# Kernel optimization log

Hardware: AMD Instinct MI355X
Metric: run time of the kernel (lower is better)

The kernel has to match this reference:

```python
import jax, jax.numpy as jnp
import numpy as np

B, N, D, H = 2, 2048, 1024, 16
HD = D // H

def setup_inputs() -> dict:
    key = jax.random.key(0)
    ks = jax.random.split(key, 8)
    s = lambda fan_in: 1.0 / np.sqrt(fan_in)
    return {
        "x": jax.random.normal(ks[0], (B, N, D), jnp.float32),
        "coverage": jax.random.uniform(ks[1], (B, N, 1), jnp.float32),
        "w_qkv": jax.random.normal(ks[2], (D, 3 * D), jnp.float32) * s(D),
        "w_out": jax.random.normal(ks[3], (D, D), jnp.float32) * s(D),
        "b_out": jnp.zeros((D,), jnp.float32),
        "w_ce1": jax.random.normal(ks[4], (1, D // 4), jnp.float32),
        "b_ce1": jnp.zeros((D // 4,), jnp.float32),
        "w_ce2": jax.random.normal(ks[5], (D // 4, H), jnp.float32) * s(D // 4),
        "b_ce2": jnp.zeros((H,), jnp.float32),
        "w_fg1": jax.random.normal(ks[6], (D, D // 4), jnp.float32) * s(D),
        "b_fg1": jnp.zeros((D // 4,), jnp.float32),
        "w_fg2": jax.random.normal(ks[7], (D // 4, 1), jnp.float32) * s(D // 4),
        "b_fg2": jnp.zeros((1,), jnp.float32),
    }

def reference(x, coverage, w_qkv, w_out, b_out, w_ce1, b_ce1, w_ce2, b_ce2,
              w_fg1, b_fg1, w_fg2, b_fg2):
    b, n, d = x.shape
    h = w_ce2.shape[1]
    hd = d // h
    scale = hd ** -0.5
    qkv = x @ w_qkv  # (B,N,3D)
    q, k, v = jnp.split(qkv, 3, axis=-1)
    q = q.reshape(b, n, h, hd).transpose(0, 2, 1, 3)  # (B,H,N,hd)
    k = k.reshape(b, n, h, hd).transpose(0, 2, 1, 3)
    v = v.reshape(b, n, h, hd).transpose(0, 2, 1, 3)
    attn = jnp.einsum("bhnd,bhmd->bhnm", q, k) * scale  # (B,H,N,N)
    # coverage bias: MLP(1 -> D/4 -> H), broadcast over query dim
    cov = jax.nn.silu(coverage @ w_ce1 + b_ce1) @ w_ce2 + b_ce2  # (B,N,H)
    cov_bias = cov.transpose(0, 2, 1)[:, :, None, :]  # (B,H,1,N)
    # fusion gate on mean-pooled features
    x_pooled = x.mean(axis=1)  # (B,D)
    g = jax.nn.sigmoid(jax.nn.silu(x_pooled @ w_fg1 + b_fg1) @ w_fg2 + b_fg2)  # (B,1)
    g = g[:, :, None, None]  # (B,1,1,1)
    # g*(attn+bias) + (1-g)*attn == attn + g*bias (exact same math)
    attn = attn + g * cov_bias
    attn = jax.nn.softmax(attn, axis=-1)
    out = jnp.einsum("bhnm,bhmd->bhnd", attn, v)  # (B,H,N,hd)
    out = out.transpose(0, 2, 1, 3).reshape(b, n, d)
    return out @ w_out + b_out
```

## Files before the change

### kernel.cpp

```cpp
#include <hip/hip_runtime.h>
#include <math.h>

typedef __bf16 bf16_t;
typedef __bf16 bf16x8 __attribute__((ext_vector_type(8)));
typedef __bf16 bf16x4 __attribute__((ext_vector_type(4)));
typedef float f32x4 __attribute__((ext_vector_type(4)));

#define MFMA16(a, b, c) __builtin_amdgcn_mfma_f32_16x16x32_bf16((a), (b), (c), 0, 0, 0)

constexpr int Bc = 2, Nc = 2048, Dc = 1024, Hc = 16, HDc = 64;
constexpr float C1 = 0.18033688011112042f;
constexpr float LOG2E = 1.4426950408889634f;

__device__ __forceinline__ void glds16(const bf16_t* g, bf16_t* l) {
    __builtin_amdgcn_global_load_lds(
        (const __attribute__((address_space(1))) unsigned int*)g,
        (__attribute__((address_space(3))) unsigned int*)l, 16, 0, 0);
}

__device__ __forceinline__ void glds4(const float* g, float* l) {
    __builtin_amdgcn_global_load_lds(
        (const __attribute__((address_space(1))) unsigned int*)g,
        (__attribute__((address_space(3))) unsigned int*)l, 4, 0, 0);
}

__global__ __launch_bounds__(256) void f2b(const float* __restrict__ src,
                                           bf16_t* __restrict__ dst) {
    int i = (blockIdx.x * 256 + threadIdx.x) * 4;
    float4 v = *(const float4*)(src + i);
    bf16x4 o = { (bf16_t)v.x, (bf16_t)v.y, (bf16_t)v.z, (bf16_t)v.w };
    *(bf16x4*)(dst + i) = o;
}

__global__ __launch_bounds__(256) void tr64(const float* __restrict__ src,
                                            bf16_t* __restrict__ dst, int R, int C) {
    __shared__ bf16_t tile[64 * 66];
    int r0 = blockIdx.y * 64, c0 = blockIdx.x * 64;
    int t = threadIdx.x;
    int cl = t & 63, rl = t >> 6;
#pragma unroll
    for (int p = 0; p < 16; ++p) {
        int r = p * 4 + rl;
        tile[r * 66 + cl] = (bf16_t)src[(size_t)(r0 + r) * C + c0 + cl];
    }
    __syncthreads();
#pragma unroll
    for (int p = 0; p < 16; ++p) {
        int r = p * 4 + rl;
        dst[(size_t)(c0 + r) * R + r0 + cl] = tile[cl * 66 + r];
    }
}

__global__ __launch_bounds__(256) void pool_partial(const float* __restrict__ x,
                                                    float* __restrict__ pooled) {
    int blk = blockIdx.x;
    int b = blk >> 7, ch = blk & 127;
    int t = threadIdx.x;
    int c = t * 4;
    float s0 = 0.f, s1 = 0.f, s2 = 0.f, s3 = 0.f;
    for (int rr = 0; rr < 16; ++rr) {
        float4 v = *(const float4*)(x + (size_t)(b * Nc + ch * 16 + rr) * Dc + c);
        s0 += v.x; s1 += v.y; s2 += v.z; s3 += v.w;
    }
    atomicAdd(&pooled[b * Dc + c + 0], s0);
    atomicAdd(&pooled[b * Dc + c + 1], s1);
    atomicAdd(&pooled[b * Dc + c + 2], s2);
    atomicAdd(&pooled[b * Dc + c + 3], s3);
}

__global__ __launch_bounds__(256) void gate1(const float* __restrict__ pooled,
                                             const float* __restrict__ w_fg1,
                                             const float* __restrict__ b_fg1,
                                             const float* __restrict__ w_fg2,
                                             float* __restrict__ hacc) {
    int b = blockIdx.x >> 8, j = blockIdx.x & 255;
    int t = threadIdx.x;
    float p = 0.f;
#pragma unroll
    for (int i = 0; i < 4; ++i) {
        int d = t * 4 + i;
        p += pooled[b * 1024 + d] * w_fg1[d * 256 + j];
    }
#pragma unroll
    for (int off = 32; off > 0; off >>= 1) p += __shfl_down(p, off);
    __shared__ float red[4];
    if ((t & 63) == 0) red[t >> 6] = p;
    __syncthreads();
    if (t == 0) {
        float hj = (red[0] + red[1] + red[2] + red[3]) * (1.0f / 2048.0f) + b_fg1[j];
        hj = hj / (1.0f + __expf(-hj));
        atomicAdd(&hacc[b], hj * w_fg2[j]);
    }
}

__global__ __launch_bounds__(256) void covbias_k(const float* __restrict__ coverage,
                                                 const float* __restrict__ w_ce1,
                                                 const float* __restrict__ b_ce1,
                                                 const float* __restrict__ w_ce2,
                                                 const float* __restrict__ b_ce2,
                                                 const float* __restrict__ hacc,
                                                 const float* __restrict__ b_fg2,
                                                 float* __restrict__ biasbuf) {
    int t = threadIdx.x;
    int h = t & 15;
    int gn = blockIdx.x * 16 + (t >> 4);
    int b = gn >> 11, n = gn & 2047;
    float g = 1.0f / (1.0f + __expf(-(hacc[b] + b_fg2[0])));
    float c = coverage[gn];
    float acc = b_ce2[h];
    for (int j = 0; j < 256; ++j) {
        float tv = c * w_ce1[j] + b_ce1[j];
        tv = tv / (1.0f + __expf(-tv));
        acc += tv * w_ce2[j * 16 + h];
    }
    biasbuf[((size_t)b * 16 + h) * 2048 + n] = LOG2E * g * acc;
}

__global__ __launch_bounds__(256) void qkv_gemm(const bf16_t* __restrict__ Xb,
                                                const bf16_t* __restrict__ Wt,
                                                bf16_t* __restrict__ Q,
                                                bf16_t* __restrict__ Kb,
                                                bf16_t* __restrict__ Vt) {
    __shared__ __align__(16) bf16_t At[128 * 32];
    __shared__ __align__(16) bf16_t Bt[128 * 32];
    int t = threadIdx.x, w = t >> 6, lane = t & 63;
    int l16 = lane & 15, quad = lane >> 4;
    int wm = w & 1, wx = w >> 1;
    int m0 = blockIdx.x * 128;
    int n0 = blockIdx.y * 128;
    f32x4 acc[4][4] = {};
    int sw = (l16 >> 2) & 3;

    for (int k0 = 0; k0 < 1024; k0 += 32) {
#pragma unroll
        for (int i = 0; i < 2; ++i) {
            int fb = i * 4096 + w * 1024;
            int f = fb + lane * 16;
            int row = f >> 6;
            int ch = (f >> 4) & 3;
            int sc = ch ^ ((row >> 2) & 3);
            glds16(Wt + (size_t)(n0 + row) * 1024 + k0 + sc * 8, At + (fb >> 1));
            glds16(Xb + (size_t)(m0 + row) * 1024 + k0 + sc * 8, Bt + (fb >> 1));
        }
        __syncthreads();
        bf16x8 afr[4], bfr[4];
#pragma unroll
        for (int mi = 0; mi < 4; ++mi)
            afr[mi] = *(const bf16x8*)(At + (wm * 64 + mi * 16 + l16) * 32 + ((quad ^ sw) * 8));
#pragma unroll
        for (int ni = 0; ni < 4; ++ni)
            bfr[ni] = *(const bf16x8*)(Bt + (wx * 64 + ni * 16 + l16) * 32 + ((quad ^ sw) * 8));
#pragma unroll
        for (int mi = 0; mi < 4; ++mi)
#pragma unroll
            for (int ni = 0; ni < 4; ++ni)
                acc[mi][ni] = MFMA16(afr[mi], bfr[ni], acc[mi][ni]);
        __syncthreads();
    }

    int sec = n0 >> 10;
    float scq = (sec == 0) ? C1 : 1.0f;
#pragma unroll
    for (int mi = 0; mi < 4; ++mi) {
        int gc = n0 + wm * 64 + mi * 16 + quad * 4;
        int dcol = gc & 1023;
        int h = dcol >> 6, hd = dcol & 63;
#pragma unroll
        for (int ni = 0; ni < 4; ++ni) {
            int gx = m0 + wx * 64 + ni * 16 + l16;
            int b = gx >> 11, n = gx & 2047;
            size_t bh = (size_t)(b * 16 + h);
            if (sec == 2) {
#pragma unroll
                for (int r = 0; r < 4; ++r)
                    Vt[(bh * 64 + hd + r) * 2048 + n] = (bf16_t)acc[mi][ni][r];
            } else {
                bf16x4 pk = { (bf16_t)(acc[mi][ni][0] * scq), (bf16_t)(acc[mi][ni][1] * scq),
                              (bf16_t)(acc[mi][ni][2] * scq), (bf16_t)(acc[mi][ni][3] * scq) };
                bf16_t* dst = (sec == 0 ? Q : Kb);
                *(bf16x4*)(dst + (bh * 2048 + n) * 64 + hd) = pk;
            }
        }
    }
}

__global__ __launch_bounds__(256) void attn_k(const bf16_t* __restrict__ Q,
                                              const bf16_t* __restrict__ Kb,
                                              const bf16_t* __restrict__ Vt,
                                              const float* __restrict__ biasbuf,
                                              bf16_t* __restrict__ O) {
    __shared__ __align__(16) bf16_t kbuf[2][64 * 64];
    __shared__ __align__(16) bf16_t vbuf[2][64 * 64];
    __shared__ __align__(16) float bbias[2][64];
    int t = threadIdx.x, w = t >> 6, lane = t & 63;
    int l16 = lane & 15, quad = lane >> 4;
    int bh = blockIdx.y;
    int b = bh >> 4, h = bh & 15;
    int qa = blockIdx.x * 128 + w * 32;
    const bf16_t* Qh = Q + (size_t)bh * 2048 * 64;
    const bf16_t* Kh = Kb + (size_t)bh * 2048 * 64;
    const bf16_t* Vh = Vt + (size_t)bh * 64 * 2048;
    const float* bih = biasbuf + (size_t)bh * 2048;

    int fb0 = w * 2048, fb1 = fb0 + 1024;
    int f0 = fb0 + lane * 16, f1 = fb1 + lane * 16;
    int krow0 = f0 >> 7, kch0 = ((f0 >> 4) & 7) ^ (krow0 & 7);
    int krow1 = f1 >> 7, kch1 = ((f1 >> 4) & 7) ^ (krow1 & 7);

    bf16x8 qf[2][2];
#pragma unroll
    for (int qt = 0; qt < 2; ++qt)
#pragma unroll
        for (int dh = 0; dh < 2; ++dh)
            qf[qt][dh] = *(const bf16x8*)(Qh + (size_t)(qa + qt * 16 + l16) * 64 + dh * 32 + quad * 8);

    f32x4 o[2][4] = {};
    f32x4 lacc[2] = {};
    bf16x8 onesb;
#pragma unroll
    for (int i = 0; i < 8; ++i) onesb[i] = (bf16_t)1.0f;
    int swl = l16 & 7;
    int qh = quad >> 1, ql = quad & 1;

    auto stage = [&](int tile, int bf) {
        int jn = tile * 64;
        glds16(Kh + (size_t)(jn + krow0) * 64 + kch0 * 8, &kbuf[bf][fb0 >> 1]);
        glds16(Kh + (size_t)(jn + krow1) * 64 + kch1 * 8, &kbuf[bf][fb1 >> 1]);
        glds16(Vh + (size_t)krow0 * 2048 + jn + kch0 * 8, &vbuf[bf][fb0 >> 1]);
        glds16(Vh + (size_t)krow1 * 2048 + jn + kch1 * 8, &vbuf[bf][fb1 >> 1]);
        glds4(bih + jn + lane, &bbias[bf][0]);
    };

    stage(0, 0);

    for (int it = 0; it < 32; ++it) {
        int sel = it & 1;
        asm volatile("s_waitcnt lgkmcnt(0)" ::: "memory");
        __builtin_amdgcn_s_barrier();
        if (it + 1 < 32) {
            stage(it + 1, sel ^ 1);
            asm volatile("s_waitcnt vmcnt(5)" ::: "memory");
        } else {
            asm volatile("s_waitcnt vmcnt(0)" ::: "memory");
        }
        __builtin_amdgcn_s_barrier();
        __builtin_amdgcn_sched_barrier(0);

        const bf16_t* kb = kbuf[sel];
        const bf16_t* vb = vbuf[sel];
        const float* bp = bbias[sel];

        f32x4 s[2][4];
        __builtin_amdgcn_s_setprio(1);
#pragma unroll
        for (int kt = 0; kt < 4; ++kt) {
            f32x4 bi = *(const f32x4*)(bp + kt * 16 + quad * 4);
            bf16x8 kf0 = *(const bf16x8*)(kb + (kt * 16 + l16) * 64 + ((quad ^ swl) * 8));
            bf16x8 kf1 = *(const bf16x8*)(kb + (kt * 16 + l16) * 64 + (((4 + quad) ^ swl) * 8));
#pragma unroll
            for (int qt = 0; qt < 2; ++qt) {
                s[qt][kt] = MFMA16(kf0, qf[qt][0], bi);
                s[qt][kt] = MFMA16(kf1, qf[qt][1], s[qt][kt]);
            }
        }
        __builtin_amdgcn_s_setprio(0);

        bf16x8 pf[2][2];
#pragma unroll
        for (int qt = 0; qt < 2; ++qt) {
#pragma unroll
            for (int kt = 0; kt < 4; ++kt)
#pragma unroll
                for (int r = 0; r < 4; ++r)
                    s[qt][kt][r] = __builtin_amdgcn_exp2f(s[qt][kt][r]);
#pragma unroll
            for (int pv = 0; pv < 2; ++pv) {
                bf16x8 tmp;
#pragma unroll
                for (int i = 0; i < 4; ++i) {
                    tmp[i]     = (bf16_t)s[qt][2 * pv][i];
                    tmp[i + 4] = (bf16_t)s[qt][2 * pv + 1][i];
                }
                pf[qt][pv] = tmp;
            }
        }

        __builtin_amdgcn_s_setprio(1);
#pragma unroll
        for (int qt = 0; qt < 2; ++qt) {
            lacc[qt] = MFMA16(pf[qt][0], onesb, lacc[qt]);
            lacc[qt] = MFMA16(pf[qt][1], onesb, lacc[qt]);
        }
#pragma unroll
        for (int dt = 0; dt < 4; ++dt) {
            const bf16_t* vrow = vb + (dt * 16 + l16) * 64 + ql * 4;
#pragma unroll
            for (int pv = 0; pv < 2; ++pv) {
                int c0 = (pv * 4 + qh) ^ swl;
                int c1 = (pv * 4 + 2 + qh) ^ swl;
                bf16x4 va = *(const bf16x4*)(vrow + c0 * 8);
                bf16x4 vc = *(const bf16x4*)(vrow + c1 * 8);
                bf16x8 vf = __builtin_shufflevector(va, vc, 0, 1, 2, 3, 4, 5, 6, 7);
#pragma unroll
                for (int qt = 0; qt < 2; ++qt)
                    o[qt][dt] = MFMA16(pf[qt][pv], vf, o[qt][dt]);
            }
        }
        __builtin_amdgcn_s_setprio(0);
    }

#pragma unroll
    for (int qt = 0; qt < 2; ++qt) {
        f32x4 rinv;
#pragma unroll
        for (int r = 0; r < 4; ++r) rinv[r] = 1.0f / lacc[qt][r];
#pragma unroll
        for (int dt = 0; dt < 4; ++dt)
#pragma unroll
            for (int r = 0; r < 4; ++r) {
                int row = qa + qt * 16 + quad * 4 + r;
                O[(size_t)(b * 2048 + row) * 1024 + h * 64 + dt * 16 + l16] =
                    (bf16_t)(o[qt][dt][r] * rinv[r]);
            }
    }
}

__global__ __launch_bounds__(256) void out_gemm(const bf16_t* __restrict__ A,
                                                const bf16_t* __restrict__ Wt,
                                                const float* __restrict__ bias,
                                                float* __restrict__ Cout) {
    __shared__ __align__(16) bf16_t At[128 * 32];
    __shared__ __align__(16) bf16_t Bt[128 * 32];
    int t = threadIdx.x, w = t >> 6, lane = t & 63;
    int l16 = lane & 15, quad = lane >> 4;
    int wm = w & 1, wx = w >> 1;
    int m0 = blockIdx.x * 128;
    int n0 = blockIdx.y * 128;
    f32x4 acc[4][4] = {};
    int sw = (l16 >> 2) & 3;

    for (int k0 = 0; k0 < 1024; k0 += 32) {
#pragma unroll
        for (int i = 0; i < 2; ++i) {
            int fb = i * 4096 + w * 1024;
            int f = fb + lane * 16;
            int row = f >> 6;
            int ch = (f >> 4) & 3;
            int sc = ch ^ ((row >> 2) & 3);
            glds16(Wt + (size_t)(n0 + row) * 1024 + k0 + sc * 8, At + (fb >> 1));
            glds16(A + (size_t)(m0 + row) * 1024 + k0 + sc * 8, Bt + (fb >> 1));
        }
        __syncthreads();
        bf16x8 afr[4], bfr[4];
#pragma unroll
        for (int mi = 0; mi < 4; ++mi)
            afr[mi] = *(const bf16x8*)(At + (wm * 64 + mi * 16 + l16) * 32 + ((quad ^ sw) * 8));
#pragma unroll
        for (int ni = 0; ni < 4; ++ni)
            bfr[ni] = *(const bf16x8*)(Bt + (wx * 64 + ni * 16 + l16) * 32 + ((quad ^ sw) * 8));
#pragma unroll
        for (int mi = 0; mi < 4; ++mi)
#pragma unroll
            for (int ni = 0; ni < 4; ++ni)
                acc[mi][ni] = MFMA16(afr[mi], bfr[ni], acc[mi][ni]);
        __syncthreads();
    }

#pragma unroll
    for (int mi = 0; mi < 4; ++mi) {
        int gc = n0 + wm * 64 + mi * 16 + quad * 4;
        float4 bv = *(const float4*)(bias + gc);
#pragma unroll
        for (int ni = 0; ni < 4; ++ni) {
            int gx = m0 + wx * 64 + ni * 16 + l16;
            float4 ov = { acc[mi][ni][0] + bv.x, acc[mi][ni][1] + bv.y,
                          acc[mi][ni][2] + bv.z, acc[mi][ni][3] + bv.w };
            *(float4*)(Cout + (size_t)gx * 1024 + gc) = ov;
        }
    }
}

extern "C" void kernel_launch(void* const* d_in, const int* in_sizes, int n_in,
                              void* d_out, int out_size, void* d_ws, size_t ws_size,
                              hipStream_t stream) {
    const float* x     = (const float*)d_in[0];
    const float* cov   = (const float*)d_in[1];
    const float* w_qkv = (const float*)d_in[2];
    const float* w_out = (const float*)d_in[3];
    const float* b_out = (const float*)d_in[4];
    const float* w_ce1 = (const float*)d_in[5];
    const float* b_ce1 = (const float*)d_in[6];
    const float* w_ce2 = (const float*)d_in[7];
    const float* b_ce2 = (const float*)d_in[8];
    const float* w_fg1 = (const float*)d_in[9];
    const float* b_fg1 = (const float*)d_in[10];
    const float* w_fg2 = (const float*)d_in[11];
    const float* b_fg2 = (const float*)d_in[12];

    char* ws = (char*)d_ws;
    bf16_t* Wt     = (bf16_t*)(ws);
    bf16_t* WoT    = (bf16_t*)(ws + 6291456);
    bf16_t* Xb     = (bf16_t*)(ws + 8388608);
    bf16_t* Qb     = (bf16_t*)(ws + 16777216);
    bf16_t* Kbb    = (bf16_t*)(ws + 25165824);
    bf16_t* Vt     = (bf16_t*)(ws + 33554432);
    bf16_t* Ob     = (bf16_t*)(ws + 41943040);
    float*  pooled = (float*)(ws + 50331648);
    float*  hacc   = (float*)(ws + 50339840);
    float*  biasb  = (float*)(ws + 50340096);

    hipMemsetAsync(pooled, 0, 2 * 1024 * sizeof(float), stream);
    hipMemsetAsync(hacc, 0, 2 * sizeof(float), stream);
    f2b<<<4096, 256, 0, stream>>>(x, Xb);
    tr64<<<dim3(48, 16), 256, 0, stream>>>(w_qkv, Wt, 1024, 3072);
    tr64<<<dim3(16, 16), 256, 0, stream>>>(w_out, WoT, 1024, 1024);
    pool_partial<<<256, 256, 0, stream>>>(x, pooled);
    gate1<<<512, 256, 0, stream>>>(pooled, w_fg1, b_fg1, w_fg2, hacc);
    covbias_k<<<256, 256, 0, stream>>>(cov, w_ce1, b_ce1, w_ce2, b_ce2, hacc, b_fg2, biasb);
    qkv_gemm<<<dim3(32, 24), 256, 0, stream>>>(Xb, Wt, Qb, Kbb, Vt);
    attn_k<<<dim3(16, 32), 256, 0, stream>>>(Qb, Kbb, Vt, biasb, Ob);
    out_gemm<<<dim3(32, 8), 256, 0, stream>>>(Ob, WoT, b_out, (float*)d_out);
}
```

Measured before the change: 261.6 us.

## Fuse prep kernels, fold gate into qkv GEMM, shrink attention blocks

Merges the bf16 cast, both weight transposes, pooling and coverage-bias MLP into one prep launch. The gate MLP now runs as an extra row of blocks in the QKV GEMM grid, and the gate scalar is applied inside attention instead of being baked into the bias. Attention moves to 128-thread blocks covering 64 queries each, which doubles the grid, adds more loads per thread and precomputes swizzled LDS offsets. The aim is to cut launch overhead and raise attention occupancy. Relying on hacc being zeroed by the widened memset (8200 bytes covers pooled plus hacc) is a subtle layout dependence.

```diff
diff --git a/kernel.cpp b/kernel.cpp
--- a/kernel.cpp
+++ b/kernel.cpp
@@ -24,19 +24,10 @@
         (__attribute__((address_space(3))) unsigned int*)l, 4, 0, 0);
 }
 
-__global__ __launch_bounds__(256) void f2b(const float* __restrict__ src,
-                                           bf16_t* __restrict__ dst) {
-    int i = (blockIdx.x * 256 + threadIdx.x) * 4;
-    float4 v = *(const float4*)(src + i);
-    bf16x4 o = { (bf16_t)v.x, (bf16_t)v.y, (bf16_t)v.z, (bf16_t)v.w };
-    *(bf16x4*)(dst + i) = o;
-}
-
-__global__ __launch_bounds__(256) void tr64(const float* __restrict__ src,
-                                            bf16_t* __restrict__ dst, int R, int C) {
-    __shared__ bf16_t tile[64 * 66];
-    int r0 = blockIdx.y * 64, c0 = blockIdx.x * 64;
-    int t = threadIdx.x;
+__device__ __forceinline__ void tr64_body(const float* __restrict__ src,
+                                          bf16_t* __restrict__ dst, int R, int C,
+                                          int bx, int by, bf16_t* tile, int t) {
+    int r0 = by * 64, c0 = bx * 64;
     int cl = t & 63, rl = t >> 6;
 #pragma unroll
     for (int p = 0; p < 16; ++p) {
@@ -51,79 +42,102 @@
     }
 }
 
-__global__ __launch_bounds__(256) void pool_partial(const float* __restrict__ x,
-                                                    float* __restrict__ pooled) {
-    int blk = blockIdx.x;
-    int b = blk >> 7, ch = blk & 127;
-    int t = threadIdx.x;
-    int c = t * 4;
-    float s0 = 0.f, s1 = 0.f, s2 = 0.f, s3 = 0.f;
-    for (int rr = 0; rr < 16; ++rr) {
-        float4 v = *(const float4*)(x + (size_t)(b * Nc + ch * 16 + rr) * Dc + c);
-        s0 += v.x; s1 += v.y; s2 += v.z; s3 += v.w;
-    }
-    atomicAdd(&pooled[b * Dc + c + 0], s0);
-    atomicAdd(&pooled[b * Dc + c + 1], s1);
-    atomicAdd(&pooled[b * Dc + c + 2], s2);
-    atomicAdd(&pooled[b * Dc + c + 3], s3);
-}
-
-__global__ __launch_bounds__(256) void gate1(const float* __restrict__ pooled,
-                                             const float* __restrict__ w_fg1,
-                                             const float* __restrict__ b_fg1,
-                                             const float* __restrict__ w_fg2,
-                                             float* __restrict__ hacc) {
-    int b = blockIdx.x >> 8, j = blockIdx.x & 255;
-    int t = threadIdx.x;
-    float p = 0.f;
-#pragma unroll
-    for (int i = 0; i < 4; ++i) {
-        int d = t * 4 + i;
-        p += pooled[b * 1024 + d] * w_fg1[d * 256 + j];
-    }
-#pragma unroll
-    for (int off = 32; off > 0; off >>= 1) p += __shfl_down(p, off);
-    __shared__ float red[4];
-    if ((t & 63) == 0) red[t >> 6] = p;
-    __syncthreads();
-    if (t == 0) {
-        float hj = (red[0] + red[1] + red[2] + red[3]) * (1.0f / 2048.0f) + b_fg1[j];
-        hj = hj / (1.0f + __expf(-hj));
-        atomicAdd(&hacc[b], hj * w_fg2[j]);
-    }
-}
-
-__global__ __launch_bounds__(256) void covbias_k(const float* __restrict__ coverage,
-                                                 const float* __restrict__ w_ce1,
-                                                 const float* __restrict__ b_ce1,
-                                                 const float* __restrict__ w_ce2,
-                                                 const float* __restrict__ b_ce2,
-                                                 const float* __restrict__ hacc,
-                                                 const float* __restrict__ b_fg2,
-                                                 float* __restrict__ biasbuf) {
-    int t = threadIdx.x;
-    int h = t & 15;
-    int gn = blockIdx.x * 16 + (t >> 4);
-    int b = gn >> 11, n = gn & 2047;
-    float g = 1.0f / (1.0f + __expf(-(hacc[b] + b_fg2[0])));
-    float c = coverage[gn];
-    float acc = b_ce2[h];
-    for (int j = 0; j < 256; ++j) {
-        float tv = c * w_ce1[j] + b_ce1[j];
-        tv = tv / (1.0f + __expf(-tv));
-        acc += tv * w_ce2[j * 16 + h];
-    }
-    biasbuf[((size_t)b * 16 + h) * 2048 + n] = LOG2E * g * acc;
+__global__ __launch_bounds__(256) void prep(const float* __restrict__ x,
+                                            bf16_t* __restrict__ Xb,
+                                            const float* __restrict__ w_qkv,
+                                            bf16_t* __restrict__ Wt,
+                                            const float* __restrict__ w_out,
+                                            bf16_t* __restrict__ WoT,
+                                            float* __restrict__ pooled,
+                                            const float* __restrict__ coverage,
+                                            const float* __restrict__ w_ce1,
+                                            const float* __restrict__ b_ce1,
+                                            const float* __restrict__ w_ce2,
+                                            const float* __restrict__ b_ce2,
+                                            float* __restrict__ cbias) {
+    __shared__ bf16_t tile[64 * 66];
+    int bid = blockIdx.x, t = threadIdx.x;
+    if (bid < 4096) {
+        int i = (bid * 256 + t) * 4;
+        float4 v = *(const float4*)(x + i);
+        bf16x4 o = { (bf16_t)v.x, (bf16_t)v.y, (bf16_t)v.z, (bf16_t)v.w };
+        *(bf16x4*)(Xb + i) = o;
+    } else if (bid < 4864) {
+        int bb = bid - 4096;
+        tr64_body(w_qkv, Wt, 1024, 3072, bb % 48, bb / 48, tile, t);
+    } else if (bid < 5120) {
+        int bb = bid - 4864;
+        tr64_body(w_out, WoT, 1024, 1024, bb & 15, bb >> 4, tile, t);
+    } else if (bid < 5376) {
+        int blk = bid - 5120;
+        int b = blk >> 7, ch = blk & 127;
+        int c = t * 4;
+        float s0 = 0.f, s1 = 0.f, s2 = 0.f, s3 = 0.f;
+        for (int rr = 0; rr < 16; ++rr) {
+            float4 v = *(const float4*)(x + (size_t)(b * Nc + ch * 16 + rr) * Dc + c);
+            s0 += v.x; s1 += v.y; s2 += v.z; s3 += v.w;
+        }
+        atomicAdd(&pooled[b * Dc + c + 0], s0);
+        atomicAdd(&pooled[b * Dc + c + 1], s1);
+        atomicAdd(&pooled[b * Dc + c + 2], s2);
+        atomicAdd(&pooled[b * Dc + c + 3], s3);
+    } else {
+        int blk = bid - 5376;
+        int h = t & 15;
+        int gn = blk * 16 + (t >> 4);
+        int b = gn >> 11, n = gn & 2047;
+        float c = coverage[gn];
+        float acc = b_ce2[h];
+        for (int j = 0; j < 256; ++j) {
+            float tv = c * w_ce1[j] + b_ce1[j];
+            tv = tv / (1.0f + __expf(-tv));
+            acc += tv * w_ce2[j * 16 + h];
+        }
+        cbias[((size_t)b * 16 + h) * 2048 + n] = LOG2E * acc;
+    }
 }
 
 __global__ __launch_bounds__(256) void qkv_gemm(const bf16_t* __restrict__ Xb,
                                                 const bf16_t* __restrict__ Wt,
                                                 bf16_t* __restrict__ Q,
                                                 bf16_t* __restrict__ Kb,
-                                                bf16_t* __restrict__ Vt) {
+                                                bf16_t* __restrict__ Vt,
+                                                const float* __restrict__ pooled,
+                                                const float* __restrict__ w_fg1,
+                                                const float* __restrict__ b_fg1,
+                                                const float* __restrict__ w_fg2,
+                                                float* __restrict__ hacc) {
     __shared__ __align__(16) bf16_t At[128 * 32];
     __shared__ __align__(16) bf16_t Bt[128 * 32];
-    int t = threadIdx.x, w = t >> 6, lane = t & 63;
+    int t = threadIdx.x;
+
+    if (blockIdx.y == 24) {
+        __shared__ float red[4];
+        int blk = blockIdx.x;
+        int b = blk >> 4, jb = (blk & 15) * 16;
+        for (int jj = 0; jj < 16; ++jj) {
+            int j = jb + jj;
+            float p = 0.f;
+#pragma unroll
+            for (int i = 0; i < 4; ++i) {
+                int d = t * 4 + i;
+                p += pooled[b * 1024 + d] * w_fg1[d * 256 + j];
+            }
+#pragma unroll
+            for (int off = 32; off > 0; off >>= 1) p += __shfl_down(p, off);
+            if ((t & 63) == 0) red[t >> 6] = p;
+            __syncthreads();
+            if (t == 0) {
+                float hj = (red[0] + red[1] + red[2] + red[3]) * (1.0f / 2048.0f) + b_fg1[j];
+                hj = hj / (1.0f + __expf(-hj));
+                atomicAdd(&hacc[b], hj * w_fg2[j]);
+            }
+            __syncthreads();
+        }
+        return;
+    }
+
+    int w = t >> 6, lane = t & 63;
     int l16 = lane & 15, quad = lane >> 4;
     int wm = w & 1, wx = w >> 1;
     int m0 = blockIdx.x * 128;
@@ -184,10 +198,12 @@
     }
 }
 
-__global__ __launch_bounds__(256) void attn_k(const bf16_t* __restrict__ Q,
+__global__ __launch_bounds__(128) void attn_k(const bf16_t* __restrict__ Q,
                                               const bf16_t* __restrict__ Kb,
                                               const bf16_t* __restrict__ Vt,
-                                              const float* __restrict__ biasbuf,
+                                              const float* __restrict__ cbias,
+                                              const float* __restrict__ hacc,
+                                              const float* __restrict__ b_fg2,
                                               bf16_t* __restrict__ O) {
     __shared__ __align__(16) bf16_t kbuf[2][64 * 64];
     __shared__ __align__(16) bf16_t vbuf[2][64 * 64];
@@ -196,16 +212,21 @@
     int l16 = lane & 15, quad = lane >> 4;
     int bh = blockIdx.y;
     int b = bh >> 4, h = bh & 15;
-    int qa = blockIdx.x * 128 + w * 32;
+    int qa = blockIdx.x * 64 + w * 32;
     const bf16_t* Qh = Q + (size_t)bh * 2048 * 64;
     const bf16_t* Kh = Kb + (size_t)bh * 2048 * 64;
     const bf16_t* Vh = Vt + (size_t)bh * 64 * 2048;
-    const float* bih = biasbuf + (size_t)bh * 2048;
-
-    int fb0 = w * 2048, fb1 = fb0 + 1024;
-    int f0 = fb0 + lane * 16, f1 = fb1 + lane * 16;
-    int krow0 = f0 >> 7, kch0 = ((f0 >> 4) & 7) ^ (krow0 & 7);
-    int krow1 = f1 >> 7, kch1 = ((f1 >> 4) & 7) ^ (krow1 & 7);
+    const float* bih = cbias + (size_t)bh * 2048;
+    float g = 1.0f / (1.0f + __expf(-(hacc[b] + b_fg2[0])));
+
+    int krow[4], ksc[4];
+#pragma unroll
+    for (int c = 0; c < 4; ++c) {
+        int f = w * 4096 + c * 1024 + lane * 16;
+        int row = f >> 7, ch = (f >> 4) & 7;
+        krow[c] = row;
+        ksc[c] = ch ^ (row & 7);
+    }
 
     bf16x8 qf[2][2];
 #pragma unroll
@@ -222,12 +243,23 @@
     int swl = l16 & 7;
     int qh = quad >> 1, ql = quad & 1;
 
-    auto stage = [&](int tile, int bf) {
-        int jn = tile * 64;
-        glds16(Kh + (size_t)(jn + krow0) * 64 + kch0 * 8, &kbuf[bf][fb0 >> 1]);
-        glds16(Kh + (size_t)(jn + krow1) * 64 + kch1 * 8, &kbuf[bf][fb1 >> 1]);
-        glds16(Vh + (size_t)krow0 * 2048 + jn + kch0 * 8, &vbuf[bf][fb0 >> 1]);
-        glds16(Vh + (size_t)krow1 * 2048 + jn + kch1 * 8, &vbuf[bf][fb1 >> 1]);
+    int bk0 = l16 * 64 + ((quad ^ swl) * 8);
+    int bk1 = l16 * 64 + (((4 + quad) ^ swl) * 8);
+    int bv0 = l16 * 64 + ql * 4 + ((qh ^ swl) * 8);
+    int bv1 = l16 * 64 + ql * 4 + (((2 + qh) ^ swl) * 8);
+    int bv2 = l16 * 64 + ql * 4 + (((4 + qh) ^ swl) * 8);
+    int bv3 = l16 * 64 + ql * 4 + (((6 + qh) ^ swl) * 8);
+
+    auto stage = [&](int tile_, int bf) {
+        int jn = tile_ * 64;
+        bf16_t* kd = &kbuf[bf][w * 2048];
+        bf16_t* vd = &vbuf[bf][w * 2048];
+#pragma unroll
+        for (int c = 0; c < 4; ++c)
+            glds16(Kh + (size_t)(jn + krow[c]) * 64 + ksc[c] * 8, kd + c * 512);
+#pragma unroll
+        for (int c = 0; c < 4; ++c)
+            glds16(Vh + (size_t)krow[c] * 2048 + jn + ksc[c] * 8, vd + c * 512);
         glds4(bih + jn + lane, &bbias[bf][0]);
     };
 
@@ -239,24 +271,25 @@
         __builtin_amdgcn_s_barrier();
         if (it + 1 < 32) {
             stage(it + 1, sel ^ 1);
-            asm volatile("s_waitcnt vmcnt(5)" ::: "memory");
+            asm volatile("s_waitcnt vmcnt(9)" ::: "memory");
         } else {
             asm volatile("s_waitcnt vmcnt(0)" ::: "memory");
         }
         __builtin_amdgcn_s_barrier();
         __builtin_amdgcn_sched_barrier(0);
 
-        const bf16_t* kb = kbuf[sel];
-        const bf16_t* vb = vbuf[sel];
-        const float* bp = bbias[sel];
+        const bf16_t* kb = &kbuf[sel][0];
+        const bf16_t* vb = &vbuf[sel][0];
+        const float* bp = &bbias[sel][0];
 
         f32x4 s[2][4];
         __builtin_amdgcn_s_setprio(1);
 #pragma unroll
         for (int kt = 0; kt < 4; ++kt) {
-            f32x4 bi = *(const f32x4*)(bp + kt * 16 + quad * 4);
-            bf16x8 kf0 = *(const bf16x8*)(kb + (kt * 16 + l16) * 64 + ((quad ^ swl) * 8));
-            bf16x8 kf1 = *(const bf16x8*)(kb + (kt * 16 + l16) * 64 + (((4 + quad) ^ swl) * 8));
+            f32x4 bv = *(const f32x4*)(bp + kt * 16 + quad * 4);
+            f32x4 bi = { bv[0] * g, bv[1] * g, bv[2] * g, bv[3] * g };
+            bf16x8 kf0 = *(const bf16x8*)(kb + kt * 1024 + bk0);
+            bf16x8 kf1 = *(const bf16x8*)(kb + kt * 1024 + bk1);
 #pragma unroll
             for (int qt = 0; qt < 2; ++qt) {
                 s[qt][kt] = MFMA16(kf0, qf[qt][0], bi);
@@ -293,17 +326,16 @@
         }
 #pragma unroll
         for (int dt = 0; dt < 4; ++dt) {
-            const bf16_t* vrow = vb + (dt * 16 + l16) * 64 + ql * 4;
-#pragma unroll
-            for (int pv = 0; pv < 2; ++pv) {
-                int c0 = (pv * 4 + qh) ^ swl;
-                int c1 = (pv * 4 + 2 + qh) ^ swl;
-                bf16x4 va = *(const bf16x4*)(vrow + c0 * 8);
-                bf16x4 vc = *(const bf16x4*)(vrow + c1 * 8);
-                bf16x8 vf = __builtin_shufflevector(va, vc, 0, 1, 2, 3, 4, 5, 6, 7);
-#pragma unroll
-                for (int qt = 0; qt < 2; ++qt)
-                    o[qt][dt] = MFMA16(pf[qt][pv], vf, o[qt][dt]);
+            bf16x4 va0 = *(const bf16x4*)(vb + dt * 1024 + bv0);
+            bf16x4 vc0 = *(const bf16x4*)(vb + dt * 1024 + bv1);
+            bf16x8 vf0 = __builtin_shufflevector(va0, vc0, 0, 1, 2, 3, 4, 5, 6, 7);
+            bf16x4 va1 = *(const bf16x4*)(vb + dt * 1024 + bv2);
+            bf16x4 vc1 = *(const bf16x4*)(vb + dt * 1024 + bv3);
+            bf16x8 vf1 = __builtin_shufflevector(va1, vc1, 0, 1, 2, 3, 4, 5, 6, 7);
+#pragma unroll
+            for (int qt = 0; qt < 2; ++qt) {
+                o[qt][dt] = MFMA16(pf[qt][0], vf0, o[qt][dt]);
+                o[qt][dt] = MFMA16(pf[qt][1], vf1, o[qt][dt]);
             }
         }
         __builtin_amdgcn_s_setprio(0);
@@ -409,15 +441,11 @@
     float*  hacc   = (float*)(ws + 50339840);
     float*  biasb  = (float*)(ws + 50340096);
 
-    hipMemsetAsync(pooled, 0, 2 * 1024 * sizeof(float), stream);
-    hipMemsetAsync(hacc, 0, 2 * sizeof(float), stream);
-    f2b<<<4096, 256, 0, stream>>>(x, Xb);
-    tr64<<<dim3(48, 16), 256, 0, stream>>>(w_qkv, Wt, 1024, 3072);
-    tr64<<<dim3(16, 16), 256, 0, stream>>>(w_out, WoT, 1024, 1024);
-    pool_partial<<<256, 256, 0, stream>>>(x, pooled);
-    gate1<<<512, 256, 0, stream>>>(pooled, w_fg1, b_fg1, w_fg2, hacc);
-    covbias_k<<<256, 256, 0, stream>>>(cov, w_ce1, b_ce1, w_ce2, b_ce2, hacc, b_fg2, biasb);
-    qkv_gemm<<<dim3(32, 24), 256, 0, stream>>>(Xb, Wt, Qb, Kbb, Vt);
-    attn_k<<<dim3(16, 32), 256, 0, stream>>>(Qb, Kbb, Vt, biasb, Ob);
+    hipMemsetAsync(pooled, 0, 8200, stream);
+    prep<<<5632, 256, 0, stream>>>(x, Xb, w_qkv, Wt, w_out, WoT, pooled,
+                                   cov, w_ce1, b_ce1, w_ce2, b_ce2, biasb);
+    qkv_gemm<<<dim3(32, 25), 256, 0, stream>>>(Xb, Wt, Qb, Kbb, Vt,
+                                               pooled, w_fg1, b_fg1, w_fg2, hacc);
+    attn_k<<<dim3(32, 32), 128, 0, stream>>>(Qb, Kbb, Vt, biasb, hacc, b_fg2, Ob);
     out_gemm<<<dim3(32, 8), 256, 0, stream>>>(Ob, WoT, b_out, (float*)d_out);
 }
```

New measurement: 267.1 us. 2.1% more time.
